# Performance work log

Hardware: AMD Instinct MI355X
Metric: run time of the kernel (lower is better)

The kernel has to match this reference:

```python
import jax, jax.numpy as jnp
import numpy as np

SCALE = 0.2  # scale init arg, clipped to [0,1]


def _relative_corners(rank):
    # [2**rank, rank] matrix of +-1 corner coordinates
    return jnp.array([[float(int(c)) * 2.0 - 1.0 for c in format(i, '0%db' % rank)]
                      for i in range(2 ** rank)], dtype=jnp.float32)


def _affine_from_noise(random_u):
    # random_u: [B, 2**r, r] uniform(0,1) -> random_scale uniform(1-SCALE, 1)
    B, n, r = random_u.shape
    out_c = _relative_corners(r)                                  # [2^r, r]
    random_scale = (1.0 - SCALE) + SCALE * random_u
    src = out_c[None] * random_scale                              # [B, 2^r, r]
    ones_col = jnp.ones((B, n, 1), jnp.float32)
    A = jnp.broadcast_to(
        jnp.concatenate([out_c, jnp.ones((n, 1), jnp.float32)], -1)[None],
        (B, n, r + 1))                                            # output corners (homog.)
    Bmat = jnp.concatenate([src, ones_col], -1)                   # source corners (homog.)
    # least-squares solve A X = B  (matrix_solve_ls): X = (A^T A)^{-1} A^T B
    AtA = jnp.einsum('bni,bnj->bij', A, A)
    AtB = jnp.einsum('bni,bnj->bij', A, Bmat)
    X = jnp.linalg.solve(AtA, AtB)                                # [B, r+1, r+1]
    return jnp.transpose(X, (0, 2, 1))                            # transform, [B, r+1, r+1]


def _make_grid(transform, spatial_shape):
    # AffineGridWarper: output voxel coords normalized to [-1,1], affine-mapped,
    # then converted to source pixel coordinates [0, size-1].
    r = len(spatial_shape)
    axes = [jnp.linspace(-1.0, 1.0, s) for s in spatial_shape]
    mesh = jnp.stack(jnp.meshgrid(*axes, indexing='ij'), -1)      # [D,H,W,r]
    mesh_h = jnp.concatenate(
        [mesh, jnp.ones(tuple(spatial_shape) + (1,), jnp.float32)], -1)
    coords = jnp.einsum('dhwj,bij->bdhwi', mesh_h, transform[:, :r, :])  # [B,D,H,W,r]
    sizes = jnp.array(spatial_shape, jnp.float32)
    return (coords + 1.0) * (sizes - 1.0) * 0.5                   # pixel coords


def _resample_linear_zero(img, coords):
    # trilinear interpolation with zero boundary: out-of-range corners contribute 0
    # img: [B,D,H,W,C], coords: [B,D,H,W,3] (pixel coordinates)
    B = img.shape[0]
    sp = jnp.array(img.shape[1:4], jnp.int32)
    f = jnp.floor(coords)
    frac = coords - f                                             # [B,D,H,W,3]
    i0 = f.astype(jnp.int32)
    bidx = jnp.arange(B)[:, None, None, None]
    out = jnp.zeros(img.shape, img.dtype)
    for corner in range(8):  # fixed structural loop over 2^3 interpolation corners
        off = jnp.array([(corner >> 2) & 1, (corner >> 1) & 1, corner & 1], jnp.int32)
        idx = i0 + off
        valid = jnp.all((idx >= 0) & (idx < sp), axis=-1)         # [B,D,H,W]
        ci = jnp.clip(idx, 0, sp - 1)
        vals = img[bidx, ci[..., 0], ci[..., 1], ci[..., 2]]      # [B,D,H,W,C]
        w = jnp.prod(jnp.where(off == 1, frac, 1.0 - frac), axis=-1)
        w = w * valid.astype(img.dtype)
        out = out + vals * w[..., None]
    return out


def setup_inputs() -> dict:
    key = jax.random.key(0)
    k1, k2 = jax.random.split(key)
    input_tensor = jax.random.normal(k1, (8, 128, 128, 128, 1), dtype=jnp.float32)
    random_u = jax.random.uniform(k2, (8, 8, 3), dtype=jnp.float32)
    return {"input_tensor": input_tensor, "random_u": random_u}


def reference(input_tensor, random_u):
    transform = _affine_from_noise(random_u)                      # [B,4,4]
    grid = _make_grid(transform, input_tensor.shape[1:4])         # [B,D,H,W,3]
    return _resample_linear_zero(input_tensor, grid)
```

## Files before the change

### kernel.cpp

```cpp
#include <hip/hip_runtime.h>

#define NB   8
#define NS   128
#define VOX  (NS*NS*NS)

#define SD    13
#define SH    13
#define ROW_W 40
#define RST   (SH*ROW_W)

typedef __attribute__((address_space(1))) const void gconst_t;
typedef __attribute__((address_space(3))) void lds_t;

__global__ __launch_bounds__(256) void warp_resample_kernel(
        const float* __restrict__ img, const float* __restrict__ u,
        float* __restrict__ out) {
    __shared__ float tm[12];
    __shared__ __align__(16) float slab[SD * RST];

    const int tid  = threadIdx.x;
    const int bi   = blockIdx.x;
    const int wblk =  bi       & 3;
    const int hblk = (bi >> 2) & 15;
    const int dblk = (bi >> 6) & 15;
    const int b    =  bi >> 10;

    if (tid < 12) {
        int i = tid >> 2, j = tid & 3;
        float acc = 0.f;
#pragma unroll
        for (int n = 0; n < 8; ++n) {
            float ci = (n & (4 >> i)) ? 1.f : -1.f;
            float cj = (j < 3) ? ((n & (4 >> j)) ? 1.f : -1.f) : 1.f;
            float s  = 0.8f + 0.2f * u[(b * 8 + n) * 3 + i];
            acc += cj * ci * s;
        }
        tm[tid] = acc * 0.125f;
    }
    __syncthreads();

    const float t00 = tm[0], t01 = tm[1], t02 = tm[2],  t03 = tm[3];
    const float t10 = tm[4], t11 = tm[5], t12 = tm[6],  t13 = tm[7];
    const float t20 = tm[8], t21 = tm[9], t22 = tm[10], t23 = tm[11];

    const int d0 = dblk << 3, h0 = hblk << 3, w0 = wblk << 5;
    const float inv = 2.0f / 127.0f;
    const float x0 = -1.f + d0 * inv, y0 = -1.f + h0 * inv, z0 = -1.f + w0 * inv;
    const float P0 = (t00 * x0 + t01 * y0 + t02 * z0 + t03 + 1.f) * 63.5f;
    const float P1 = (t10 * x0 + t11 * y0 + t12 * z0 + t13 + 1.f) * 63.5f;
    const float P2 = (t20 * x0 + t21 * y0 + t22 * z0 + t23 + 1.f) * 63.5f;

    const float mn0 = P0 + fminf(0.f, 7.f*t00) + fminf(0.f, 7.f*t01) + fminf(0.f, 31.f*t02);
    const float mx0 = P0 + fmaxf(0.f, 7.f*t00) + fmaxf(0.f, 7.f*t01) + fmaxf(0.f, 31.f*t02);
    const float mn1 = P1 + fminf(0.f, 7.f*t10) + fminf(0.f, 7.f*t11) + fminf(0.f, 31.f*t12);
    const float mx1 = P1 + fmaxf(0.f, 7.f*t10) + fmaxf(0.f, 7.f*t11) + fmaxf(0.f, 31.f*t12);
    const float mn2 = P2 + fminf(0.f, 7.f*t20) + fminf(0.f, 7.f*t21) + fminf(0.f, 31.f*t22);
    const float mx2 = P2 + fmaxf(0.f, 7.f*t20) + fmaxf(0.f, 7.f*t21) + fmaxf(0.f, 31.f*t22);

    const int i0mn = (int)floorf(mn0), i0mx = (int)floorf(mx0);
    const int i1mn = (int)floorf(mn1), i1mx = (int)floorf(mx1);
    const int i2mn = (int)floorf(mn2), i2mx = (int)floorf(mx2);

    const int d_lo = i0mn;
    const int h_lo = i1mn;
    const int ws   = (i2mn - 1) & ~3;
    const int Sd   = min(i0mx + 2 - d_lo, SD);
    const int Sh   = min(i1mx + 2 - h_lo, SH);

    const int allin = __builtin_amdgcn_readfirstlane(
        (d_lo >= 0 && d_lo + Sd <= NS &&
         h_lo >= 0 && h_lo + Sh <= NS &&
         ws   >= 0 && ws + ROW_W <= NS) ? 1 : 0);
    const int off = __builtin_amdgcn_readfirstlane(
        -(d_lo * RST + h_lo * ROW_W + ws));

    if (!allin) {
        float4* p = (float4*)slab;
        for (int i = tid; i < (SD * RST) / 4; i += 256)
            p[i] = make_float4(0.f, 0.f, 0.f, 0.f);
        __syncthreads();
    }

    {
        const float* gb = img + (size_t)b * VOX;
        const int hi = tid / 10;
        const int c  = tid - hi * 10;
        const int wvbase = (tid & ~63) << 2;
        if (allin) {
            if (hi < Sh) {
                for (int di = 0; di < Sd; ++di) {
                    const float* g = gb + (((d_lo + di) * NS + (h_lo + hi)) * NS
                                           + ws + (c << 2));
                    __builtin_amdgcn_global_load_lds(
                        (gconst_t*)g, (lds_t*)(slab + di * RST + wvbase), 16, 0, 0);
                }
            }
        } else {
            const int  cc = ws + (c << 2);
            const bool ok = (hi < Sh) && ((unsigned)(h_lo + hi) < NS)
                                      && ((unsigned)cc <= NS - 4);
            if (ok) {
                for (int di = 0; di < Sd; ++di) {
                    if ((unsigned)(d_lo + di) < NS) {
                        const float* g = gb + (((d_lo + di) * NS + (h_lo + hi)) * NS
                                               + cc);
                        __builtin_amdgcn_global_load_lds(
                            (gconst_t*)g, (lds_t*)(slab + di * RST + wvbase), 16, 0, 0);
                    }
                }
            }
        }
    }
    __syncthreads();

    const int wl = tid & 31, hh = tid >> 5;
    float q0 = P0 + hh * t01 + wl * t02;
    float q1 = P1 + hh * t11 + wl * t12;
    float q2 = P2 + hh * t21 + wl * t22;

    float res[8];
#pragma unroll
    for (int k = 0; k < 8; ++k) {
        float f0 = floorf(q0), f1 = floorf(q1), f2 = floorf(q2);
        int   i0 = (int)f0,    i1 = (int)f1,    i2 = (int)f2;
        float r0 = q0 - f0,    r1 = q1 - f1,    r2 = q2 - f2;

        int base = i0 * RST + i1 * ROW_W + i2 + off;
        float a00 = slab[base],           b00 = slab[base + 1];
        float a01 = slab[base + ROW_W],   b01 = slab[base + ROW_W + 1];
        int base2 = base + RST;
        float a10 = slab[base2],          b10 = slab[base2 + 1];
        float a11 = slab[base2 + ROW_W],  b11 = slab[base2 + ROW_W + 1];

        float e0 = fmaf(r2, b00 - a00, a00);
        float e1 = fmaf(r2, b01 - a01, a01);
        float e2 = fmaf(r2, b10 - a10, a10);
        float e3 = fmaf(r2, b11 - a11, a11);
        float c0 = fmaf(r1, e1 - e0, e0);
        float c1 = fmaf(r1, e3 - e2, e2);
        res[k] = fmaf(r0, c1 - c0, c0);

        q0 += t00; q1 += t10; q2 += t20;
    }

    size_t ob = (((size_t)(b * NS + d0) * NS + (h0 + hh)) * NS) + w0 + wl;
#pragma unroll
    for (int k = 0; k < 8; ++k)
        out[ob + (size_t)k * NS * NS] = res[k];
}

extern "C" void kernel_launch(void* const* d_in, const int* in_sizes, int n_in,
                              void* d_out, int out_size, void* d_ws, size_t ws_size,
                              hipStream_t stream) {
    const float* img = (const float*)d_in[0];
    const float* u   = (const float*)d_in[1];
    float* out = (float*)d_out;

    int blocks = NB * 16 * 16 * 4;
    warp_resample_kernel<<<blocks, 256, 0, stream>>>(img, u, out);
}
```

Baseline: 122.1 us.

## Double-buffer LDS slabs across four w-tiles per block with prefetch

Each block now handles four consecutive w-tiles instead of one and keeps two LDS slab buffers, so the next tile's global-to-LDS load is issued before the current tile is interpolated. The affine transform is computed per thread in registers, which drops the shared-memory table and one barrier. Block indices are remapped in groups of eight to change scheduling locality across XCDs. This cuts the grid to a quarter of its size and doubles LDS use per block, which can lower occupancy. It also adds an extra barrier per tile.

After: 130.9 us. +7.2%, slower.

```diff
diff --git a/kernel.cpp b/kernel.cpp
--- a/kernel.cpp
+++ b/kernel.cpp
@@ -8,6 +8,7 @@
 #define SH    13
 #define ROW_W 40
 #define RST   (SH*ROW_W)
+#define SLAB  (SD*RST)
 
 typedef __attribute__((address_space(1))) const void gconst_t;
 typedef __attribute__((address_space(3))) void lds_t;
@@ -15,138 +16,169 @@
 __global__ __launch_bounds__(256) void warp_resample_kernel(
         const float* __restrict__ img, const float* __restrict__ u,
         float* __restrict__ out) {
-    __shared__ float tm[12];
-    __shared__ __align__(16) float slab[SD * RST];
+    __shared__ __align__(16) float slab[2 * SLAB];
 
-    const int tid  = threadIdx.x;
-    const int bi   = blockIdx.x;
-    const int wblk =  bi       & 3;
-    const int hblk = (bi >> 2) & 15;
-    const int dblk = (bi >> 6) & 15;
-    const int b    =  bi >> 10;
+    const int tid = threadIdx.x;
+    int bi = blockIdx.x;
+    bi = (bi & 7) * 256 + (bi >> 3);
+    const int hblk = bi & 15;
+    const int dblk = (bi >> 4) & 15;
+    const int b    = bi >> 8;
 
-    if (tid < 12) {
-        int i = tid >> 2, j = tid & 3;
-        float acc = 0.f;
+    const float* ub = u + b * 24;
+    float T[3][4];
+#pragma unroll
+    for (int i = 0; i < 3; ++i) {
+        float v[8];
 #pragma unroll
         for (int n = 0; n < 8; ++n) {
-            float ci = (n & (4 >> i)) ? 1.f : -1.f;
-            float cj = (j < 3) ? ((n & (4 >> j)) ? 1.f : -1.f) : 1.f;
-            float s  = 0.8f + 0.2f * u[(b * 8 + n) * 3 + i];
-            acc += cj * ci * s;
+            const float sg = (n & (4 >> i)) ? 1.f : -1.f;
+            v[n] = fmaf(sg * 0.025f, ub[n * 3 + i], sg * 0.1f);
         }
-        tm[tid] = acc * 0.125f;
+        const float a0 = v[0] + v[1], a1 = v[2] + v[3];
+        const float a2 = v[4] + v[5], a3 = v[6] + v[7];
+        const float d0 = v[1] - v[0], d1 = v[3] - v[2];
+        const float d2 = v[5] - v[4], d3 = v[7] - v[6];
+        const float A01 = a0 + a1, A23 = a2 + a3;
+        T[i][0] = A23 - A01;
+        T[i][1] = (a1 - a0) + (a3 - a2);
+        T[i][2] = (d0 + d1) + (d2 + d3);
+        T[i][3] = A01 + A23;
     }
-    __syncthreads();
+    const float t00 = T[0][0], t01 = T[0][1], t02 = T[0][2], t03 = T[0][3];
+    const float t10 = T[1][0], t11 = T[1][1], t12 = T[1][2], t13 = T[1][3];
+    const float t20 = T[2][0], t21 = T[2][1], t22 = T[2][2], t23 = T[2][3];
 
-    const float t00 = tm[0], t01 = tm[1], t02 = tm[2],  t03 = tm[3];
-    const float t10 = tm[4], t11 = tm[5], t12 = tm[6],  t13 = tm[7];
-    const float t20 = tm[8], t21 = tm[9], t22 = tm[10], t23 = tm[11];
+    const int d0i = dblk << 3, h0i = hblk << 3;
+    const float inv = 2.0f / 127.0f;
+    const float x0 = -1.f + d0i * inv, y0 = -1.f + h0i * inv;
 
-    const int d0 = dblk << 3, h0 = hblk << 3, w0 = wblk << 5;
-    const float inv = 2.0f / 127.0f;
-    const float x0 = -1.f + d0 * inv, y0 = -1.f + h0 * inv, z0 = -1.f + w0 * inv;
-    const float P0 = (t00 * x0 + t01 * y0 + t02 * z0 + t03 + 1.f) * 63.5f;
-    const float P1 = (t10 * x0 + t11 * y0 + t12 * z0 + t13 + 1.f) * 63.5f;
-    const float P2 = (t20 * x0 + t21 * y0 + t22 * z0 + t23 + 1.f) * 63.5f;
+    const int wl = tid & 31, hh = tid >> 5;
 
-    const float mn0 = P0 + fminf(0.f, 7.f*t00) + fminf(0.f, 7.f*t01) + fminf(0.f, 31.f*t02);
-    const float mx0 = P0 + fmaxf(0.f, 7.f*t00) + fmaxf(0.f, 7.f*t01) + fmaxf(0.f, 31.f*t02);
-    const float mn1 = P1 + fminf(0.f, 7.f*t10) + fminf(0.f, 7.f*t11) + fminf(0.f, 31.f*t12);
-    const float mx1 = P1 + fmaxf(0.f, 7.f*t10) + fmaxf(0.f, 7.f*t11) + fmaxf(0.f, 31.f*t12);
-    const float mn2 = P2 + fminf(0.f, 7.f*t20) + fminf(0.f, 7.f*t21) + fminf(0.f, 31.f*t22);
-    const float mx2 = P2 + fmaxf(0.f, 7.f*t20) + fmaxf(0.f, 7.f*t21) + fmaxf(0.f, 31.f*t22);
+    const int hi     = tid / 10;
+    const int cch    = tid - hi * 10;
+    const int wvbase = (tid & ~63) << 2;
+    const float* gb  = img + (size_t)b * VOX;
 
-    const int i0mn = (int)floorf(mn0), i0mx = (int)floorf(mx0);
-    const int i1mn = (int)floorf(mn1), i1mx = (int)floorf(mx1);
-    const int i2mn = (int)floorf(mn2), i2mx = (int)floorf(mx2);
+    int   c_dlo = 0, c_hlo = 0, c_ws = 0, c_Sd = 0, c_Sh = 0, c_allin = 1;
+    float c_Pl0 = 0.f, c_Pl1 = 0.f, c_Pl2 = 0.f;
+    int   n_dlo = 0, n_hlo = 0, n_ws = 0, n_Sd = 0, n_Sh = 0, n_allin = 1;
+    float n_Pl0 = 0.f, n_Pl1 = 0.f, n_Pl2 = 0.f;
 
-    const int d_lo = i0mn;
-    const int h_lo = i1mn;
-    const int ws   = (i2mn - 1) & ~3;
-    const int Sd   = min(i0mx + 2 - d_lo, SD);
-    const int Sh   = min(i1mx + 2 - h_lo, SH);
+    auto bounds = [&](int w0t, int& dlo, int& hlo, int& ws, int& Sdv, int& Shv,
+                      int& allin, float& Pl0, float& Pl1, float& Pl2) {
+        const float z0 = -1.f + w0t * inv;
+        const float P0 = (t00 * x0 + t01 * y0 + t02 * z0 + t03 + 1.f) * 63.5f;
+        const float P1 = (t10 * x0 + t11 * y0 + t12 * z0 + t13 + 1.f) * 63.5f;
+        const float P2 = (t20 * x0 + t21 * y0 + t22 * z0 + t23 + 1.f) * 63.5f;
+        const float mn0 = P0 + fminf(0.f,7.f*t00)+fminf(0.f,7.f*t01)+fminf(0.f,31.f*t02);
+        const float mx0 = P0 + fmaxf(0.f,7.f*t00)+fmaxf(0.f,7.f*t01)+fmaxf(0.f,31.f*t02);
+        const float mn1 = P1 + fminf(0.f,7.f*t10)+fminf(0.f,7.f*t11)+fminf(0.f,31.f*t12);
+        const float mx1 = P1 + fmaxf(0.f,7.f*t10)+fmaxf(0.f,7.f*t11)+fmaxf(0.f,31.f*t12);
+        const float mn2 = P2 + fminf(0.f,7.f*t20)+fminf(0.f,7.f*t21)+fminf(0.f,31.f*t22);
+        const float mx2 = P2 + fmaxf(0.f,7.f*t20)+fmaxf(0.f,7.f*t21)+fmaxf(0.f,31.f*t22);
+        const int i0mn = (int)floorf(mn0), i0mx = (int)floorf(mx0);
+        const int i1mn = (int)floorf(mn1), i1mx = (int)floorf(mx1);
+        const int i2mn = (int)floorf(mn2), i2mx = (int)floorf(mx2);
+        dlo = i0mn;
+        hlo = i1mn;
+        ws  = (i2mn - 1) & ~3;
+        Sdv = min(i0mx + 2 - dlo, SD);
+        Shv = min(i1mx + 2 - hlo, SH);
+        allin = __builtin_amdgcn_readfirstlane(
+            (dlo >= 0 && dlo + Sdv <= NS && hlo >= 0 && hlo + Shv <= NS &&
+             ws >= 0 && ws + ROW_W <= NS) ? 1 : 0);
+        Pl0 = P0 - (float)dlo; Pl1 = P1 - (float)hlo; Pl2 = P2 - (float)ws;
+    };
 
-    const int allin = __builtin_amdgcn_readfirstlane(
-        (d_lo >= 0 && d_lo + Sd <= NS &&
-         h_lo >= 0 && h_lo + Sh <= NS &&
-         ws   >= 0 && ws + ROW_W <= NS) ? 1 : 0);
-    const int off = __builtin_amdgcn_readfirstlane(
-        -(d_lo * RST + h_lo * ROW_W + ws));
+    auto zerofill = [&](int bsel) {
+        float4* p = (float4*)(slab + bsel * SLAB);
+        for (int i = tid; i < SLAB / 4; i += 256)
+            p[i] = make_float4(0.f, 0.f, 0.f, 0.f);
+    };
 
-    if (!allin) {
-        float4* p = (float4*)slab;
-        for (int i = tid; i < (SD * RST) / 4; i += 256)
-            p[i] = make_float4(0.f, 0.f, 0.f, 0.f);
-        __syncthreads();
-    }
-
-    {
-        const float* gb = img + (size_t)b * VOX;
-        const int hi = tid / 10;
-        const int c  = tid - hi * 10;
-        const int wvbase = (tid & ~63) << 2;
+    auto stage = [&](int bsel, int dlo, int hlo, int ws, int Sdv, int Shv,
+                     int allin) {
+        float* dst0 = slab + bsel * SLAB;
         if (allin) {
-            if (hi < Sh) {
-                for (int di = 0; di < Sd; ++di) {
-                    const float* g = gb + (((d_lo + di) * NS + (h_lo + hi)) * NS
-                                           + ws + (c << 2));
+            if (hi < Shv) {
+                for (int di = 0; di < Sdv; ++di) {
+                    const float* g = gb + (((dlo + di) * NS + (hlo + hi)) * NS
+                                           + ws + (cch << 2));
                     __builtin_amdgcn_global_load_lds(
-                        (gconst_t*)g, (lds_t*)(slab + di * RST + wvbase), 16, 0, 0);
+                        (gconst_t*)g, (lds_t*)(dst0 + di * RST + wvbase), 16, 0, 0);
                 }
             }
         } else {
-            const int  cc = ws + (c << 2);
-            const bool ok = (hi < Sh) && ((unsigned)(h_lo + hi) < NS)
-                                      && ((unsigned)cc <= NS - 4);
+            const int  cc = ws + (cch << 2);
+            const bool ok = (hi < Shv) && ((unsigned)(hlo + hi) < NS)
+                                       && ((unsigned)cc <= NS - 4);
             if (ok) {
-                for (int di = 0; di < Sd; ++di) {
-                    if ((unsigned)(d_lo + di) < NS) {
-                        const float* g = gb + (((d_lo + di) * NS + (h_lo + hi)) * NS
-                                               + cc);
+                for (int di = 0; di < Sdv; ++di) {
+                    if ((unsigned)(dlo + di) < NS) {
+                        const float* g = gb + (((dlo + di) * NS + (hlo + hi)) * NS + cc);
                         __builtin_amdgcn_global_load_lds(
-                            (gconst_t*)g, (lds_t*)(slab + di * RST + wvbase), 16, 0, 0);
+                            (gconst_t*)g, (lds_t*)(dst0 + di * RST + wvbase), 16, 0, 0);
                     }
                 }
             }
         }
+    };
+
+    bounds(0, c_dlo, c_hlo, c_ws, c_Sd, c_Sh, c_allin, c_Pl0, c_Pl1, c_Pl2);
+    if (!c_allin) { zerofill(0); __syncthreads(); }
+    stage(0, c_dlo, c_hlo, c_ws, c_Sd, c_Sh, c_allin);
+
+    const size_t ob = (((size_t)(b * NS + d0i) * NS + (h0i + hh)) * NS) + wl;
+
+    for (int t = 0; t < 4; ++t) {
+        __syncthreads();
+
+        if (t < 3) {
+            bounds((t + 1) << 5, n_dlo, n_hlo, n_ws, n_Sd, n_Sh, n_allin,
+                   n_Pl0, n_Pl1, n_Pl2);
+            if (!n_allin) { zerofill((t + 1) & 1); __syncthreads(); }
+            stage((t + 1) & 1, n_dlo, n_hlo, n_ws, n_Sd, n_Sh, n_allin);
+        }
+
+        const float* bp = slab + (t & 1) * SLAB;
+        float ql0 = c_Pl0 + hh * t01 + wl * t02;
+        float ql1 = c_Pl1 + hh * t11 + wl * t12;
+        float ql2 = c_Pl2 + hh * t21 + wl * t22;
+
+        float res[8];
+#pragma unroll
+        for (int k = 0; k < 8; ++k) {
+            const float f0 = floorf(ql0), f1 = floorf(ql1), f2 = floorf(ql2);
+            const int   i0 = (int)f0,     i1 = (int)f1,     i2 = (int)f2;
+            const float r0 = ql0 - f0,    r1 = ql1 - f1,    r2 = ql2 - f2;
+
+            const int base = i0 * RST + i1 * ROW_W + i2;
+            float a00 = bp[base],           b00 = bp[base + 1];
+            float a01 = bp[base + ROW_W],   b01 = bp[base + ROW_W + 1];
+            const int base2 = base + RST;
+            float a10 = bp[base2],          b10 = bp[base2 + 1];
+            float a11 = bp[base2 + ROW_W],  b11 = bp[base2 + ROW_W + 1];
+
+            float e0 = fmaf(r2, b00 - a00, a00);
+            float e1 = fmaf(r2, b01 - a01, a01);
+            float e2 = fmaf(r2, b10 - a10, a10);
+            float e3 = fmaf(r2, b11 - a11, a11);
+            float c0 = fmaf(r1, e1 - e0, e0);
+            float c1 = fmaf(r1, e3 - e2, e2);
+            res[k] = fmaf(r0, c1 - c0, c0);
+
+            ql0 += t00; ql1 += t10; ql2 += t20;
+        }
+
+        const size_t obt = ob + (size_t)(t << 5);
+#pragma unroll
+        for (int k = 0; k < 8; ++k)
+            out[obt + (size_t)k * NS * NS] = res[k];
+
+        c_dlo = n_dlo; c_hlo = n_hlo; c_ws = n_ws; c_Sd = n_Sd; c_Sh = n_Sh;
+        c_allin = n_allin; c_Pl0 = n_Pl0; c_Pl1 = n_Pl1; c_Pl2 = n_Pl2;
     }
-    __syncthreads();
-
-    const int wl = tid & 31, hh = tid >> 5;
-    float q0 = P0 + hh * t01 + wl * t02;
-    float q1 = P1 + hh * t11 + wl * t12;
-    float q2 = P2 + hh * t21 + wl * t22;
-
-    float res[8];
-#pragma unroll
-    for (int k = 0; k < 8; ++k) {
-        float f0 = floorf(q0), f1 = floorf(q1), f2 = floorf(q2);
-        int   i0 = (int)f0,    i1 = (int)f1,    i2 = (int)f2;
-        float r0 = q0 - f0,    r1 = q1 - f1,    r2 = q2 - f2;
-
-        int base = i0 * RST + i1 * ROW_W + i2 + off;
-        float a00 = slab[base],           b00 = slab[base + 1];
-        float a01 = slab[base + ROW_W],   b01 = slab[base + ROW_W + 1];
-        int base2 = base + RST;
-        float a10 = slab[base2],          b10 = slab[base2 + 1];
-        float a11 = slab[base2 + ROW_W],  b11 = slab[base2 + ROW_W + 1];
-
-        float e0 = fmaf(r2, b00 - a00, a00);
-        float e1 = fmaf(r2, b01 - a01, a01);
-        float e2 = fmaf(r2, b10 - a10, a10);
-        float e3 = fmaf(r2, b11 - a11, a11);
-        float c0 = fmaf(r1, e1 - e0, e0);
-        float c1 = fmaf(r1, e3 - e2, e2);
-        res[k] = fmaf(r0, c1 - c0, c0);
-
-        q0 += t00; q1 += t10; q2 += t20;
-    }
-
-    size_t ob = (((size_t)(b * NS + d0) * NS + (h0 + hh)) * NS) + w0 + wl;
-#pragma unroll
-    for (int k = 0; k < 8; ++k)
-        out[ob + (size_t)k * NS * NS] = res[k];
 }
 
 extern "C" void kernel_launch(void* const* d_in, const int* in_sizes, int n_in,
@@ -156,6 +188,6 @@
     const float* u   = (const float*)d_in[1];
     float* out = (float*)d_out;
 
-    int blocks = NB * 16 * 16 * 4;
+    int blocks = NB * 16 * 16;
     warp_resample_kernel<<<blocks, 256, 0, stream>>>(img, u, out);
 }
```

## Compute affine transform per thread, interleave batches across blocks, slab-local coords

Applied to the files above, without the earlier changes.

Each thread now computes the 3x4 affine transform itself with a butterfly-style sum, removing the shared-memory tm array and its barrier. The block index is remapped so batch is the fastest-varying dimension, which spreads neighbouring blocks across different batch images. Sample coordinates are rebased to slab-local positions in float, which removes the integer offset add in the gather loop. The cost is redundant per-thread transform math and a different rounding path for the local coordinates.

New measurement: 122.1 us. About the same (-0.0%).

```diff
diff --git a/kernel.cpp b/kernel.cpp
--- a/kernel.cpp
+++ b/kernel.cpp
@@ -8,6 +8,7 @@
 #define SH    13
 #define ROW_W 40
 #define RST   (SH*ROW_W)
+#define SLAB  (SD*RST)
 
 typedef __attribute__((address_space(1))) const void gconst_t;
 typedef __attribute__((address_space(3))) void lds_t;
@@ -15,47 +16,53 @@
 __global__ __launch_bounds__(256) void warp_resample_kernel(
         const float* __restrict__ img, const float* __restrict__ u,
         float* __restrict__ out) {
-    __shared__ float tm[12];
-    __shared__ __align__(16) float slab[SD * RST];
+    __shared__ __align__(16) float slab[SLAB];
 
-    const int tid  = threadIdx.x;
+    const int tid = threadIdx.x;
     const int bi   = blockIdx.x;
-    const int wblk =  bi       & 3;
-    const int hblk = (bi >> 2) & 15;
-    const int dblk = (bi >> 6) & 15;
-    const int b    =  bi >> 10;
+    const int b    =  bi & 7;
+    const int idx  =  bi >> 3;
+    const int wblk =  idx & 3;
+    const int hblk = (idx >> 2) & 15;
+    const int dblk =  idx >> 6;
 
-    if (tid < 12) {
-        int i = tid >> 2, j = tid & 3;
-        float acc = 0.f;
+    const float* ub = u + b * 24;
+    float T[3][4];
+#pragma unroll
+    for (int i = 0; i < 3; ++i) {
+        float v[8];
 #pragma unroll
         for (int n = 0; n < 8; ++n) {
-            float ci = (n & (4 >> i)) ? 1.f : -1.f;
-            float cj = (j < 3) ? ((n & (4 >> j)) ? 1.f : -1.f) : 1.f;
-            float s  = 0.8f + 0.2f * u[(b * 8 + n) * 3 + i];
-            acc += cj * ci * s;
+            const float sg = (n & (4 >> i)) ? 1.f : -1.f;
+            v[n] = fmaf(sg * 0.025f, ub[n * 3 + i], sg * 0.1f);
         }
-        tm[tid] = acc * 0.125f;
+        const float a0 = v[0] + v[1], a1 = v[2] + v[3];
+        const float a2 = v[4] + v[5], a3 = v[6] + v[7];
+        const float d0 = v[1] - v[0], d1 = v[3] - v[2];
+        const float d2 = v[5] - v[4], d3 = v[7] - v[6];
+        const float A01 = a0 + a1, A23 = a2 + a3;
+        T[i][0] = A23 - A01;
+        T[i][1] = (a1 - a0) + (a3 - a2);
+        T[i][2] = (d0 + d1) + (d2 + d3);
+        T[i][3] = A01 + A23;
     }
-    __syncthreads();
+    const float t00 = T[0][0], t01 = T[0][1], t02 = T[0][2], t03 = T[0][3];
+    const float t10 = T[1][0], t11 = T[1][1], t12 = T[1][2], t13 = T[1][3];
+    const float t20 = T[2][0], t21 = T[2][1], t22 = T[2][2], t23 = T[2][3];
 
-    const float t00 = tm[0], t01 = tm[1], t02 = tm[2],  t03 = tm[3];
-    const float t10 = tm[4], t11 = tm[5], t12 = tm[6],  t13 = tm[7];
-    const float t20 = tm[8], t21 = tm[9], t22 = tm[10], t23 = tm[11];
-
-    const int d0 = dblk << 3, h0 = hblk << 3, w0 = wblk << 5;
+    const int d0i = dblk << 3, h0i = hblk << 3, w0i = wblk << 5;
     const float inv = 2.0f / 127.0f;
-    const float x0 = -1.f + d0 * inv, y0 = -1.f + h0 * inv, z0 = -1.f + w0 * inv;
+    const float x0 = -1.f + d0i * inv, y0 = -1.f + h0i * inv, z0 = -1.f + w0i * inv;
     const float P0 = (t00 * x0 + t01 * y0 + t02 * z0 + t03 + 1.f) * 63.5f;
     const float P1 = (t10 * x0 + t11 * y0 + t12 * z0 + t13 + 1.f) * 63.5f;
     const float P2 = (t20 * x0 + t21 * y0 + t22 * z0 + t23 + 1.f) * 63.5f;
 
-    const float mn0 = P0 + fminf(0.f, 7.f*t00) + fminf(0.f, 7.f*t01) + fminf(0.f, 31.f*t02);
-    const float mx0 = P0 + fmaxf(0.f, 7.f*t00) + fmaxf(0.f, 7.f*t01) + fmaxf(0.f, 31.f*t02);
-    const float mn1 = P1 + fminf(0.f, 7.f*t10) + fminf(0.f, 7.f*t11) + fminf(0.f, 31.f*t12);
-    const float mx1 = P1 + fmaxf(0.f, 7.f*t10) + fmaxf(0.f, 7.f*t11) + fmaxf(0.f, 31.f*t12);
-    const float mn2 = P2 + fminf(0.f, 7.f*t20) + fminf(0.f, 7.f*t21) + fminf(0.f, 31.f*t22);
-    const float mx2 = P2 + fmaxf(0.f, 7.f*t20) + fmaxf(0.f, 7.f*t21) + fmaxf(0.f, 31.f*t22);
+    const float mn0 = P0 + fminf(0.f,7.f*t00)+fminf(0.f,7.f*t01)+fminf(0.f,31.f*t02);
+    const float mx0 = P0 + fmaxf(0.f,7.f*t00)+fmaxf(0.f,7.f*t01)+fmaxf(0.f,31.f*t02);
+    const float mn1 = P1 + fminf(0.f,7.f*t10)+fminf(0.f,7.f*t11)+fminf(0.f,31.f*t12);
+    const float mx1 = P1 + fmaxf(0.f,7.f*t10)+fmaxf(0.f,7.f*t11)+fmaxf(0.f,31.f*t12);
+    const float mn2 = P2 + fminf(0.f,7.f*t20)+fminf(0.f,7.f*t21)+fminf(0.f,31.f*t22);
+    const float mx2 = P2 + fmaxf(0.f,7.f*t20)+fmaxf(0.f,7.f*t21)+fmaxf(0.f,31.f*t22);
 
     const int i0mn = (int)floorf(mn0), i0mx = (int)floorf(mx0);
     const int i1mn = (int)floorf(mn1), i1mx = (int)floorf(mx1);
@@ -71,12 +78,14 @@
         (d_lo >= 0 && d_lo + Sd <= NS &&
          h_lo >= 0 && h_lo + Sh <= NS &&
          ws   >= 0 && ws + ROW_W <= NS) ? 1 : 0);
-    const int off = __builtin_amdgcn_readfirstlane(
-        -(d_lo * RST + h_lo * ROW_W + ws));
+
+    const float Pl0 = P0 - (float)d_lo;
+    const float Pl1 = P1 - (float)h_lo;
+    const float Pl2 = P2 - (float)ws;
 
     if (!allin) {
         float4* p = (float4*)slab;
-        for (int i = tid; i < (SD * RST) / 4; i += 256)
+        for (int i = tid; i < SLAB / 4; i += 256)
             p[i] = make_float4(0.f, 0.f, 0.f, 0.f);
         __syncthreads();
     }
@@ -114,21 +123,21 @@
     __syncthreads();
 
     const int wl = tid & 31, hh = tid >> 5;
-    float q0 = P0 + hh * t01 + wl * t02;
-    float q1 = P1 + hh * t11 + wl * t12;
-    float q2 = P2 + hh * t21 + wl * t22;
+    float ql0 = Pl0 + hh * t01 + wl * t02;
+    float ql1 = Pl1 + hh * t11 + wl * t12;
+    float ql2 = Pl2 + hh * t21 + wl * t22;
 
     float res[8];
 #pragma unroll
     for (int k = 0; k < 8; ++k) {
-        float f0 = floorf(q0), f1 = floorf(q1), f2 = floorf(q2);
-        int   i0 = (int)f0,    i1 = (int)f1,    i2 = (int)f2;
-        float r0 = q0 - f0,    r1 = q1 - f1,    r2 = q2 - f2;
+        const float f0 = floorf(ql0), f1 = floorf(ql1), f2 = floorf(ql2);
+        const int   i0 = (int)f0,     i1 = (int)f1,     i2 = (int)f2;
+        const float r0 = ql0 - f0,    r1 = ql1 - f1,    r2 = ql2 - f2;
 
-        int base = i0 * RST + i1 * ROW_W + i2 + off;
+        const int base = i0 * RST + i1 * ROW_W + i2;
         float a00 = slab[base],           b00 = slab[base + 1];
         float a01 = slab[base + ROW_W],   b01 = slab[base + ROW_W + 1];
-        int base2 = base + RST;
+        const int base2 = base + RST;
         float a10 = slab[base2],          b10 = slab[base2 + 1];
         float a11 = slab[base2 + ROW_W],  b11 = slab[base2 + ROW_W + 1];
 
@@ -140,10 +149,10 @@
         float c1 = fmaf(r1, e3 - e2, e2);
         res[k] = fmaf(r0, c1 - c0, c0);
 
-        q0 += t00; q1 += t10; q2 += t20;
+        ql0 += t00; ql1 += t10; ql2 += t20;
     }
 
-    size_t ob = (((size_t)(b * NS + d0) * NS + (h0 + hh)) * NS) + w0 + wl;
+    size_t ob = (((size_t)(b * NS + d0i) * NS + (h0i + hh)) * NS) + w0i + wl;
 #pragma unroll
     for (int k = 0; k < 8; ++k)
         out[ob + (size_t)k * NS * NS] = res[k];
```
